# Optimization experiments

Hardware: AMD Instinct MI355X
Metric: run time of the kernel (lower is better)

Reference implementation:

```python
import jax, jax.numpy as jnp
import numpy as np

MAX_ABS = 1.0          # assumed get_max_abs('T')
DT = 0.01              # forward default dt
TWO_PI = 2.0 * np.pi
B, D, N = 4096, 2048, 4096


def setup_inputs() -> dict:
    key = jax.random.key(0)
    k0, k1 = jax.random.split(key, 2)
    x = jax.random.normal(k0, (B, D), dtype=jnp.float32)
    # nn.Linear params
    W = jax.random.normal(k1, (N, D), dtype=jnp.float32) * (1.0 / np.sqrt(D))
    b = jnp.zeros((N,), dtype=jnp.float32)
    # oscillator params (as initialized in __init__)
    amplitude = jnp.ones((N,), dtype=jnp.float32)
    frequency = jnp.ones((N,), dtype=jnp.float32)
    phase_offset = jnp.zeros((N,), dtype=jnp.float32)
    damping = jnp.full((N,), 0.01, dtype=jnp.float32)
    return {"x": x, "W": W, "b": b, "amplitude": amplitude,
            "frequency": frequency, "phase_offset": phase_offset,
            "damping": damping}


def reference(x, W, b, amplitude, frequency, phase_offset, damping):
    # driving force: [B, N]
    force = x @ W.T + b
    omega_sq = (TWO_PI * frequency) ** 2  # [N]
    # t starts at 0 and is incremented ONCE per forward call
    t = DT

    def step(carry, f):
        state, vel = carry
        accel = -omega_sq * state - damping * vel + f
        vel = vel + accel * DT
        state = state + vel * DT
        return (state, vel), state

    init = (jnp.zeros((N,), x.dtype), jnp.zeros((N,), x.dtype))
    (_, _), states = jax.lax.scan(step, init, force)  # states: [B, N]

    # sinusoid term is identical for every batch step (t fixed within forward)
    osc = amplitude * jnp.sin(TWO_PI * frequency * t + phase_offset)  # [N]
    out = jnp.clip(states + osc, -MAX_ABS, MAX_ABS)
    return out
```

## Files before the change

kernel.cpp:

```cpp
#include <hip/hip_runtime.h>
#include <hip/hip_bf16.h>
#include <math.h>

#define MDIM 4096
#define KDIM 2048
#define NDIM 4096
#define DT   0.01f
#define TWO_PI_F 6.283185307179586f
#define CH 64
#define CL 64
#define TILES (KDIM / 64)

typedef __attribute__((ext_vector_type(8))) short bf16x8;
typedef __attribute__((ext_vector_type(4))) float f32x4;

__device__ __forceinline__ unsigned short f2bf(float f) {
  unsigned int u = __float_as_uint(f);
  u += 0x7FFFu + ((u >> 16) & 1u);
  return (unsigned short)(u >> 16);
}
__device__ __forceinline__ float bf2f(unsigned short u) {
  return __uint_as_float(((unsigned int)u) << 16);
}

__global__ void cast2_bf16_kernel(const float* __restrict__ s0,
                                  unsigned short* __restrict__ d0,
                                  const float* __restrict__ s1,
                                  unsigned short* __restrict__ d1,
                                  int n4each) {
  int i = blockIdx.x * blockDim.x + threadIdx.x;
  const float4* sp;
  ushort4* dp;
  int j;
  if (i < n4each) { sp = (const float4*)s0; dp = (ushort4*)d0; j = i; }
  else            { sp = (const float4*)s1; dp = (ushort4*)d1; j = i - n4each; }
  float4 v = sp[j];
  ushort4 o;
  o.x = f2bf(v.x); o.y = f2bf(v.y); o.z = f2bf(v.z); o.w = f2bf(v.w);
  dp[j] = o;
}


__device__ __forceinline__ void gload16(const unsigned short* g,
                                        unsigned short* l) {
  __builtin_amdgcn_global_load_lds(
      (const __attribute__((address_space(1))) unsigned int*)g,
      (__attribute__((address_space(3))) unsigned int*)l, 16, 0, 0);
}

#define WAITVM(n) asm volatile("s_waitcnt vmcnt(" #n ")" ::: "memory")

__global__ __launch_bounds__(512, 2) void gemm_scan256_kernel(
    const unsigned short* __restrict__ A,
    const unsigned short* __restrict__ Bm,
    const float* __restrict__ bias,
    const float* __restrict__ freq,
    const float* __restrict__ damp,
    unsigned short* __restrict__ zpart,
    float* __restrict__ chunkS,
    float* __restrict__ chunkV) {
  extern __shared__ __align__(16) unsigned short smem[];

  const int tid  = threadIdx.x;
  const int lane = tid & 63;
  const int w    = tid >> 6;
  const int wr   = w >> 2;
  const int wc   = w & 3;
  const int q    = lane >> 4;
  const int lm   = lane & 15;

  const int bid = blockIdx.x;
  const int wg  = (bid & 7) * 32 + (bid >> 3);
  const int tm  = wg >> 4;
  const int tn  = wg & 15;
  const int bM  = tm * 256;
  const int bN  = tn * 256;

  const int srow  = w * 16 + (lane >> 2);
  const int sslot = (lane & 3) ^ ((lane >> 3) & 3);
  const unsigned short* gA = A  + (size_t)(bM + srow) * KDIM + sslot * 8;
  const unsigned short* gB = Bm + (size_t)(bN + srow) * KDIM + sslot * 8;
  const int ldst = w * 512 + lane * 8;

#define SUNIT(mat, u, ks, rh)                                              \
  gload16((mat ? gB : gA) + (size_t)(rh) * 128 * KDIM + (u) * 64 + (ks) * 32, \
          smem + ((u) & 1) * 32768 + (mat) * 16384 + (ks) * 8192 +         \
              (rh) * 4096 + ldst)

  const int flane = (lm >> 1) & 3;
  const int aoff  = (wr * 128 + lm) * 32 + ((q ^ flane) * 8);
  const int boff  = 16384 + (wc * 64 + lm) * 32 + ((q ^ flane) * 8);

  f32x4 acc[8][4];
#pragma unroll
  for (int i = 0; i < 8; i++)
#pragma unroll
    for (int j = 0; j < 4; j++) acc[i][j] = (f32x4){0.f, 0.f, 0.f, 0.f};

  SUNIT(1, 0, 0, 0); SUNIT(1, 0, 0, 1);
  SUNIT(0, 0, 0, 0); SUNIT(0, 0, 0, 1);
  SUNIT(1, 0, 1, 0); SUNIT(1, 0, 1, 1);
  SUNIT(0, 0, 1, 0); SUNIT(0, 0, 1, 1);
  SUNIT(1, 1, 0, 0); SUNIT(1, 1, 0, 1);
  SUNIT(0, 1, 0, 0); SUNIT(0, 1, 0, 1);
  SUNIT(1, 1, 1, 0); SUNIT(1, 1, 1, 1);

#define LDA(KS, MH)                                                        \
  _Pragma("unroll") for (int m = 0; m < 4; ++m) af[m] =                    \
      *(const bf16x8*)&smem[bufo + (KS) + (MH) + aoff + m * 512]
#define LDB(KS)                                                            \
  _Pragma("unroll") for (int n = 0; n < 4; ++n) bfv[n] =                   \
      *(const bf16x8*)&smem[bufo + (KS) + boff + n * 512]
#define MFMA16(MB)                                                         \
  __builtin_amdgcn_s_setprio(1);                                           \
  _Pragma("unroll") for (int m = 0; m < 4; ++m)                            \
      _Pragma("unroll") for (int n = 0; n < 4; ++n)                        \
          acc[(MB) + m][n] = __builtin_amdgcn_mfma_f32_16x16x32_bf16(      \
              af[m], bfv[n], acc[(MB) + m][n], 0, 0, 0);                   \
  __builtin_amdgcn_s_setprio(0)

#pragma unroll 2
  for (int t = 0; t < TILES; ++t) {
    const int bufo = (t & 1) * 32768;
    bf16x8 af[4], bfv[4];

    if (t < TILES - 1) WAITVM(10); else WAITVM(4);
    __builtin_amdgcn_s_barrier();
    LDA(0, 0);
    LDB(0);
    if (t + 1 < TILES) { SUNIT(0, t + 1, 1, 0); SUNIT(0, t + 1, 1, 1); }
    MFMA16(0);

    __builtin_amdgcn_s_barrier();
    LDA(0, 2048);
    if (t + 2 < TILES) { SUNIT(1, t + 2, 0, 0); SUNIT(1, t + 2, 0, 1); }
    MFMA16(4);

    if (t < TILES - 2) WAITVM(10);
    else if (t == TILES - 2) WAITVM(8);
    else WAITVM(0);
    __builtin_amdgcn_s_barrier();
    LDA(8192, 0);
    LDB(8192);
    if (t + 2 < TILES) { SUNIT(0, t + 2, 0, 0); SUNIT(0, t + 2, 0, 1); }
    MFMA16(0);

    __builtin_amdgcn_s_barrier();
    LDA(8192, 2048);
    if (t + 2 < TILES) { SUNIT(1, t + 2, 1, 0); SUNIT(1, t + 2, 1, 1); }
    MFMA16(4);
  }
#undef LDA
#undef LDB
#undef MFMA16
#undef SUNIT

  __syncthreads();

#pragma unroll
  for (int n = 0; n < 4; ++n) {
    const float bz = bias[bN + wc * 64 + n * 16 + lm];
#pragma unroll
    for (int M = 0; M < 8; ++M)
#pragma unroll
      for (int rr = 0; rr < 4; ++rr) {
        const int row = wr * 128 + M * 16 + q * 4 + rr;
        const int col = wc * 64 + ((n ^ q) * 16) + lm;
        smem[row * 256 + col] = f2bf(acc[M][n][rr] + bz);
      }
  }
  __syncthreads();

  {
    const int col  = tid & 255;
    const int ch0  = (tid >> 8) * 2;
    const int gcol = bN + col;
    const float om  = TWO_PI_F * freq[gcol];
    const float osq = om * om;
    const float dp  = damp[gcol];
#pragma unroll
    for (int cc = 0; cc < 2; ++cc) {
      const int ch = ch0 + cc;
      float s = 0.f, v = 0.f;
#pragma unroll 8
      for (int i = 0; i < CL; ++i) {
        const int row = ch * 64 + i;
        const int idx = row * 256 + (col ^ (((i >> 2) & 3) << 4));
        float f = bf2f(smem[idx]);
        v += (-osq * s - dp * v + f) * DT;
        s += v * DT;
        smem[idx] = f2bf(s);
      }
      const int chunk = tm * 4 + ch;
      chunkS[chunk * NDIM + gcol] = s;
      chunkV[chunk * NDIM + gcol] = v;
    }
  }
  __syncthreads();

#pragma unroll
  for (int k = 0; k < 16; ++k) {
    const int slot = tid + 512 * k;
    const int row  = slot >> 5;
    const int grp  = slot & 31;
    const int sgrp = grp ^ (((row >> 2) & 3) << 1);
    *(uint4*)&zpart[(size_t)(bM + row) * NDIM + bN + grp * 8] =
        *(const uint4*)&smem[row * 256 + sgrp * 8];
  }
}

__global__ void scan_pass2_inplace(float* __restrict__ chunkS,
                                   float* __restrict__ chunkV,
                                   const float* __restrict__ freq,
                                   const float* __restrict__ damp) {
  int n = blockIdx.x * blockDim.x + threadIdx.x;
  float om = TWO_PI_F * freq[n];
  float osq = om * om;
  float dp = damp[n];
  float a00 = 1.f - osq * DT * DT, a01 = DT * (1.f - dp * DT);
  float a10 = -osq * DT,           a11 = 1.f - dp * DT;
#pragma unroll
  for (int i = 0; i < 6; i++) {
    float b00 = a00 * a00 + a01 * a10;
    float b01 = a00 * a01 + a01 * a11;
    float b10 = a10 * a00 + a11 * a10;
    float b11 = a10 * a01 + a11 * a11;
    a00 = b00; a01 = b01; a10 = b10; a11 = b11;
  }
  float cs = 0.f, cv = 0.f;
#pragma unroll 8
  for (int c = 0; c < CH; c++) {
    float ls = chunkS[c * NDIM + n];
    float lv = chunkV[c * NDIM + n];
    chunkS[c * NDIM + n] = cs;
    chunkV[c * NDIM + n] = cv;
    float ns = a00 * cs + a01 * cv + ls;
    float nv = a10 * cs + a11 * cv + lv;
    cs = ns; cv = nv;
  }
}

__global__ void scan_out_carry4(const unsigned short* __restrict__ zpart,
                                const float* __restrict__ amp,
                                const float* __restrict__ freq,
                                const float* __restrict__ phase,
                                const float* __restrict__ damp,
                                const float* __restrict__ carryS,
                                const float* __restrict__ carryV,
                                float* __restrict__ out) {
  int gid = blockIdx.x * blockDim.x + threadIdx.x;
  int n4 = gid & (NDIM / 4 - 1);
  int cq = gid >> 10;
  int c  = cq >> 2;
  int qq = cq & 3;
  int n  = n4 * 4;

  float4 fr = *(const float4*)&freq[n];
  float4 dv = *(const float4*)&damp[n];
  float4 am = *(const float4*)&amp[n];
  float4 ph = *(const float4*)&phase[n];
  float omv[4] = {TWO_PI_F * fr.x, TWO_PI_F * fr.y, TWO_PI_F * fr.z, TWO_PI_F * fr.w};
  float dpv[4] = {dv.x, dv.y, dv.z, dv.w};
  float amv[4] = {am.x, am.y, am.z, am.w};
  float phv[4] = {ph.x, ph.y, ph.z, ph.w};
  float m00[4], m01[4], m10[4], m11[4], osc[4];
#pragma unroll
  for (int j = 0; j < 4; j++) {
    float osq = omv[j] * omv[j];
    m00[j] = 1.f - osq * DT * DT;  m01[j] = DT * (1.f - dpv[j] * DT);
    m10[j] = -osq * DT;            m11[j] = 1.f - dpv[j] * DT;
    osc[j] = amv[j] * sinf(omv[j] * DT + phv[j]);
  }

  float4 csv = *(const float4*)&carryS[c * NDIM + n];
  float4 cvv = *(const float4*)&carryV[c * NDIM + n];
  float cs[4] = {csv.x, csv.y, csv.z, csv.w};
  float cv[4] = {cvv.x, cvv.y, cvv.z, cvv.w};
  float hs[4], hv[4];
#pragma unroll
  for (int j = 0; j < 4; j++) {
    float p00 = m00[j], p01 = m01[j], p10 = m10[j], p11 = m11[j];
#pragma unroll
    for (int k = 0; k < 4; k++) {
      float b00 = p00 * p00 + p01 * p10;
      float b01 = p00 * p01 + p01 * p11;
      float b10 = p10 * p00 + p11 * p10;
      float b11 = p10 * p01 + p11 * p11;
      p00 = b00; p01 = b01; p10 = b10; p11 = b11;
    }
    float j00 = 1.f, j01 = 0.f, j10 = 0.f, j11 = 1.f;
    for (int k = 0; k < qq; k++) {
      float b00 = j00 * p00 + j01 * p10;
      float b01 = j00 * p01 + j01 * p11;
      float b10 = j10 * p00 + j11 * p10;
      float b11 = j10 * p01 + j11 * p11;
      j00 = b00; j01 = b01; j10 = b10; j11 = b11;
    }
    hs[j] = j00 * cs[j] + j01 * cv[j];
    hv[j] = j10 * cs[j] + j11 * cv[j];
  }

  const size_t r0 = (size_t)c * CL + qq * 16;
  const unsigned short* zp = zpart + r0 * NDIM + n;
  float* op = out + r0 * NDIM + n;
#pragma unroll 4
  for (int i = 0; i < 16; ++i) {
    ushort4 zv = *(const ushort4*)&zp[(size_t)i * NDIM];
    float z[4] = {bf2f(zv.x), bf2f(zv.y), bf2f(zv.z), bf2f(zv.w)};
    float o[4];
#pragma unroll
    for (int j = 0; j < 4; j++) {
      float t = m00[j] * hs[j] + m01[j] * hv[j];
      float u = m10[j] * hs[j] + m11[j] * hv[j];
      hs[j] = t; hv[j] = u;
      o[j] = fminf(1.f, fmaxf(-1.f, hs[j] + z[j] + osc[j]));
    }
    *(float4*)&op[(size_t)i * NDIM] = (float4){o[0], o[1], o[2], o[3]};
  }
}

__global__ __launch_bounds__(256, 2) void gemm_bt_kernel(
    const unsigned short* __restrict__ A,
    const unsigned short* __restrict__ Bm,
    const float* __restrict__ bias,
    unsigned short* __restrict__ C) {
  __shared__ __align__(16) unsigned short sA[128 * 32];
  __shared__ __align__(16) unsigned short sB[128 * 32];

  const int tid  = threadIdx.x;
  const int lane = tid & 63;
  const int wave = tid >> 6;
  const int wr = wave >> 1;
  const int wc = wave & 1;
  const int q  = lane >> 4;
  const int lm = lane & 15;

  const int bM = blockIdx.x * 128;
  const int bN = blockIdx.y * 128;

  f32x4 acc[4][4];
#pragma unroll
  for (int i = 0; i < 4; i++)
#pragma unroll
    for (int j = 0; j < 4; j++) acc[i][j] = (f32x4){0.f, 0.f, 0.f, 0.f};

  const int idx0 = tid;
  const int idx1 = tid + 256;
  const int r0 = idx0 >> 2, g0 = idx0 & 3;
  const int r1 = idx1 >> 2, g1 = idx1 & 3;
  const int dst0 = r0 * 32 + ((g0 ^ ((r0 >> 1) & 3)) * 8);
  const int dst1 = r1 * 32 + ((g1 ^ ((r1 >> 1) & 3)) * 8);
  const unsigned short* gA0 = A  + (size_t)(bM + r0) * KDIM + g0 * 8;
  const unsigned short* gA1 = A  + (size_t)(bM + r1) * KDIM + g1 * 8;
  const unsigned short* gB0 = Bm + (size_t)(bN + r0) * KDIM + g0 * 8;
  const unsigned short* gB1 = Bm + (size_t)(bN + r1) * KDIM + g1 * 8;
  const int rq = (q ^ ((lm >> 1) & 3)) * 8;

  for (int k0 = 0; k0 < KDIM; k0 += 32) {
    uint4 av0 = *(const uint4*)(gA0 + k0);
    uint4 av1 = *(const uint4*)(gA1 + k0);
    uint4 bv0 = *(const uint4*)(gB0 + k0);
    uint4 bv1 = *(const uint4*)(gB1 + k0);
    __syncthreads();
    *(uint4*)&sA[dst0] = av0;
    *(uint4*)&sA[dst1] = av1;
    *(uint4*)&sB[dst0] = bv0;
    *(uint4*)&sB[dst1] = bv1;
    __syncthreads();

    bf16x8 af[4], bfr[4];
#pragma unroll
    for (int mt = 0; mt < 4; mt++)
      af[mt]  = *(const bf16x8*)&sA[(wr * 64 + mt * 16 + lm) * 32 + rq];
#pragma unroll
    for (int nt = 0; nt < 4; nt++)
      bfr[nt] = *(const bf16x8*)&sB[(wc * 64 + nt * 16 + lm) * 32 + rq];

#pragma unroll
    for (int mt = 0; mt < 4; mt++)
#pragma unroll
      for (int nt = 0; nt < 4; nt++)
        acc[mt][nt] = __builtin_amdgcn_mfma_f32_16x16x32_bf16(
            af[mt], bfr[nt], acc[mt][nt], 0, 0, 0);
  }

#pragma unroll
  for (int nt = 0; nt < 4; nt++) {
    const int col = bN + wc * 64 + nt * 16 + lm;
    const float bz = bias[col];
#pragma unroll
    for (int mt = 0; mt < 4; mt++) {
      const int row0 = bM + wr * 64 + mt * 16 + q * 4;
#pragma unroll
      for (int r = 0; r < 4; r++)
        C[(size_t)(row0 + r) * NDIM + col] = f2bf(acc[mt][nt][r] + bz);
    }
  }
}

__global__ void scan_pass1(const unsigned short* __restrict__ force,
                           const float* __restrict__ freq,
                           const float* __restrict__ damp,
                           float* __restrict__ chunkS,
                           float* __restrict__ chunkV) {
  int gid = blockIdx.x * blockDim.x + threadIdx.x;
  int n4 = gid & (NDIM / 4 - 1);
  int c  = gid >> 10;
  int n  = n4 * 4;
  float4 fr = *(const float4*)&freq[n];
  float4 dv = *(const float4*)&damp[n];
  float osq[4] = {TWO_PI_F * fr.x, TWO_PI_F * fr.y, TWO_PI_F * fr.z, TWO_PI_F * fr.w};
  float dp[4]  = {dv.x, dv.y, dv.z, dv.w};
  float s[4] = {0.f, 0.f, 0.f, 0.f}, v[4] = {0.f, 0.f, 0.f, 0.f};
#pragma unroll
  for (int j = 0; j < 4; j++) osq[j] *= osq[j];
  const unsigned short* fp = force + (size_t)c * CL * NDIM + n;
#pragma unroll 4
  for (int i = 0; i < CL; i++) {
    ushort4 fv = *(const ushort4*)&fp[(size_t)i * NDIM];
    float f[4] = {bf2f(fv.x), bf2f(fv.y), bf2f(fv.z), bf2f(fv.w)};
#pragma unroll
    for (int j = 0; j < 4; j++) {
      float a = -osq[j] * s[j] - dp[j] * v[j] + f[j];
      v[j] += a * DT;
      s[j] += v[j] * DT;
    }
  }
  *(float4*)&chunkS[c * NDIM + n] = (float4){s[0], s[1], s[2], s[3]};
  *(float4*)&chunkV[c * NDIM + n] = (float4){v[0], v[1], v[2], v[3]};
}

__global__ void scan_pass2(const float* __restrict__ chunkS,
                           const float* __restrict__ chunkV,
                           const float* __restrict__ freq,
                           const float* __restrict__ damp,
                           float* __restrict__ carryS,
                           float* __restrict__ carryV) {
  int n = blockIdx.x * blockDim.x + threadIdx.x;
  float om = TWO_PI_F * freq[n];
  float osq = om * om;
  float dp = damp[n];
  float a00 = 1.f - osq * DT * DT, a01 = DT * (1.f - dp * DT);
  float a10 = -osq * DT,           a11 = 1.f - dp * DT;
#pragma unroll
  for (int i = 0; i < 6; i++) {
    float b00 = a00 * a00 + a01 * a10;
    float b01 = a00 * a01 + a01 * a11;
    float b10 = a10 * a00 + a11 * a10;
    float b11 = a10 * a01 + a11 * a11;
    a00 = b00; a01 = b01; a10 = b10; a11 = b11;
  }
  float cs = 0.f, cv = 0.f;
#pragma unroll 8
  for (int c = 0; c < CH; c++) {
    carryS[c * NDIM + n] = cs;
    carryV[c * NDIM + n] = cv;
    float ls = chunkS[c * NDIM + n];
    float lv = chunkV[c * NDIM + n];
    float ns = a00 * cs + a01 * cv + ls;
    float nv = a10 * cs + a11 * cv + lv;
    cs = ns; cv = nv;
  }
}

__global__ void scan_pass3(const unsigned short* __restrict__ force,
                           const float* __restrict__ amp,
                           const float* __restrict__ freq,
                           const float* __restrict__ phase,
                           const float* __restrict__ damp,
                           const float* __restrict__ carryS,
                           const float* __restrict__ carryV,
                           float* __restrict__ out) {
  int gid = blockIdx.x * blockDim.x + threadIdx.x;
  int n4 = gid & (NDIM / 4 - 1);
  int c  = gid >> 10;
  int n  = n4 * 4;
  float4 fr = *(const float4*)&freq[n];
  float4 dv = *(const float4*)&damp[n];
  float4 am = *(const float4*)&amp[n];
  float4 ph = *(const float4*)&phase[n];
  float om[4] = {TWO_PI_F * fr.x, TWO_PI_F * fr.y, TWO_PI_F * fr.z, TWO_PI_F * fr.w};
  float dp[4] = {dv.x, dv.y, dv.z, dv.w};
  float osq[4], osc[4], s[4], v[4];
  float amv[4] = {am.x, am.y, am.z, am.w};
  float phv[4] = {ph.x, ph.y, ph.z, ph.w};
#pragma unroll
  for (int j = 0; j < 4; j++) {
    osq[j] = om[j] * om[j];
    osc[j] = amv[j] * sinf(om[j] * DT + phv[j]);
  }
  float4 csv = *(const float4*)&carryS[c * NDIM + n];
  float4 cvv = *(const float4*)&carryV[c * NDIM + n];
  s[0] = csv.x; s[1] = csv.y; s[2] = csv.z; s[3] = csv.w;
  v[0] = cvv.x; v[1] = cvv.y; v[2] = cvv.z; v[3] = cvv.w;
  const unsigned short* fp = force + (size_t)c * CL * NDIM + n;
  float* op = out + (size_t)c * CL * NDIM + n;
#pragma unroll 4
  for (int i = 0; i < CL; i++) {
    ushort4 fv = *(const ushort4*)&fp[(size_t)i * NDIM];
    float f[4] = {bf2f(fv.x), bf2f(fv.y), bf2f(fv.z), bf2f(fv.w)};
    float o[4];
#pragma unroll
    for (int j = 0; j < 4; j++) {
      float a = -osq[j] * s[j] - dp[j] * v[j] + f[j];
      v[j] += a * DT;
      s[j] += v[j] * DT;
      o[j] = fminf(1.f, fmaxf(-1.f, s[j] + osc[j]));
    }
    *(float4*)&op[(size_t)i * NDIM] = (float4){o[0], o[1], o[2], o[3]};
  }
}

extern "C" void kernel_launch(void* const* d_in, const int* in_sizes, int n_in,
                              void* d_out, int out_size, void* d_ws, size_t ws_size,
                              hipStream_t stream) {
  const float* x     = (const float*)d_in[0];
  const float* W     = (const float*)d_in[1];
  const float* bias  = (const float*)d_in[2];
  const float* amp   = (const float*)d_in[3];
  const float* freq  = (const float*)d_in[4];
  const float* phase = (const float*)d_in[5];
  const float* damp  = (const float*)d_in[6];

  const size_t MiB = 1024 * 1024;
  const int n4each = MDIM * KDIM / 4;

  if (ws_size >= 66 * MiB) {
    unsigned short* xbf   = (unsigned short*)d_ws;
    unsigned short* wbf   = xbf + (size_t)MDIM * KDIM;
    unsigned short* zpart = wbf + (size_t)NDIM * KDIM;
    float* chunkS = (float*)((char*)d_ws + 64 * MiB);
    float* chunkV = chunkS + CH * NDIM;

    static bool attr_done = false;
    if (!attr_done) {
      (void)hipFuncSetAttribute((const void*)gemm_scan256_kernel,
                                hipFuncAttributeMaxDynamicSharedMemorySize,
                                131072);
      attr_done = true;
    }

    cast2_bf16_kernel<<<(2 * n4each + 255) / 256, 256, 0, stream>>>(
        x, xbf, W, wbf, n4each);
    gemm_scan256_kernel<<<dim3(256), dim3(512), 131072, stream>>>(
        xbf, wbf, bias, freq, damp, zpart, chunkS, chunkV);
    scan_pass2_inplace<<<NDIM / 256, 256, 0, stream>>>(chunkS, chunkV,
                                                       freq, damp);
    scan_out_carry4<<<CH * 4 * NDIM / 4 / 256, 256, 0, stream>>>(
        zpart, amp, freq, phase, damp, chunkS, chunkV, (float*)d_out);
  } else {
    dim3 gg(MDIM / 128, NDIM / 128);
    unsigned short* xbf   = (unsigned short*)d_ws;
    unsigned short* wbf   = xbf + (size_t)MDIM * KDIM;
    unsigned short* force = wbf + (size_t)NDIM * KDIM;
    float* chunkS = (float*)d_ws;
    float* chunkV = chunkS + CH * NDIM;
    float* carryS = chunkV + CH * NDIM;
    float* carryV = carryS + CH * NDIM;

    cast2_bf16_kernel<<<(2 * n4each + 255) / 256, 256, 0, stream>>>(
        x, xbf, W, wbf, n4each);
    gemm_bt_kernel<<<gg, 256, 0, stream>>>(xbf, wbf, bias, force);
    scan_pass1<<<CH * NDIM / 4 / 256, 256, 0, stream>>>(force, freq, damp,
                                                        chunkS, chunkV);
    scan_pass2<<<NDIM / 256, 256, 0, stream>>>(chunkS, chunkV, freq, damp,
                                               carryS, carryV);
    scan_pass3<<<CH * NDIM / 4 / 256, 256, 0, stream>>>(
        force, amp, freq, phase, damp, carryS, carryV, (float*)d_out);
  }
}
```

Baseline: 207.5 us.

## Double-buffer LDS fragments in registers to overlap ds_reads with MFMA

Restructures the GEMM main loop so the A/B fragments for the next MFMA group are read from LDS into a second register set while the current group's MFMAs execute. It uses explicit lgkmcnt waits and sched_barriers to keep the compiler from reordering. The vmcnt waits are rebalanced around the new stage layout. This hides LDS read latency but doubles fragment registers, which risks pressure at 512 threads x2 occupancy, and it makes the barrier/wait-count ordering more fragile.

After: 256.0 us. +23.3%, slower.

```diff
diff --git a/kernel.cpp b/kernel.cpp
--- a/kernel.cpp
+++ b/kernel.cpp
@@ -49,6 +49,8 @@
 }
 
 #define WAITVM(n) asm volatile("s_waitcnt vmcnt(" #n ")" ::: "memory")
+#define WAITLGKM(n) asm volatile("s_waitcnt lgkmcnt(" #n ")" ::: "memory")
+#define SCHEDB() __builtin_amdgcn_sched_barrier(0)
 
 __global__ __launch_bounds__(512, 2) void gemm_scan256_kernel(
     const unsigned short* __restrict__ A,
@@ -105,53 +107,67 @@
   SUNIT(0, 1, 0, 0); SUNIT(0, 1, 0, 1);
   SUNIT(1, 1, 1, 0); SUNIT(1, 1, 1, 1);
 
-#define LDA(KS, MH)                                                        \
-  _Pragma("unroll") for (int m = 0; m < 4; ++m) af[m] =                    \
-      *(const bf16x8*)&smem[bufo + (KS) + (MH) + aoff + m * 512]
-#define LDB(KS)                                                            \
-  _Pragma("unroll") for (int n = 0; n < 4; ++n) bfv[n] =                   \
-      *(const bf16x8*)&smem[bufo + (KS) + boff + n * 512]
-#define MFMA16(MB)                                                         \
-  __builtin_amdgcn_s_setprio(1);                                           \
+#define LDA4(dst, BUFO, KS, MH)                                            \
+  _Pragma("unroll") for (int m = 0; m < 4; ++m) dst[m] =                   \
+      *(const bf16x8*)&smem[(BUFO) + (KS) + (MH) + aoff + m * 512]
+#define LDB4(dst, BUFO, KS)                                                \
+  _Pragma("unroll") for (int n = 0; n < 4; ++n) dst[n] =                   \
+      *(const bf16x8*)&smem[(BUFO) + (KS) + boff + n * 512]
+#define MFMA16(AF, BF, MB)                                                 \
+  __builtin_amdgcn_s_setprio(1);                                          \
   _Pragma("unroll") for (int m = 0; m < 4; ++m)                            \
       _Pragma("unroll") for (int n = 0; n < 4; ++n)                        \
           acc[(MB) + m][n] = __builtin_amdgcn_mfma_f32_16x16x32_bf16(      \
-              af[m], bfv[n], acc[(MB) + m][n], 0, 0, 0);                   \
+              AF[m], BF[n], acc[(MB) + m][n], 0, 0, 0);                    \
   __builtin_amdgcn_s_setprio(0)
+
+  bf16x8 af0[4], af1[4], bf0[4], bf1[4];
+
+  WAITVM(10);
+  __builtin_amdgcn_s_barrier();
+  LDA4(af0, 0, 0, 0);
+  LDB4(bf0, 0, 0);
 
 #pragma unroll 2
   for (int t = 0; t < TILES; ++t) {
-    const int bufo = (t & 1) * 32768;
-    bf16x8 af[4], bfv[4];
-
-    if (t < TILES - 1) WAITVM(10); else WAITVM(4);
+    const int bufo  = (t & 1) * 32768;
+    const int nbufo = ((t + 1) & 1) * 32768;
+
     __builtin_amdgcn_s_barrier();
-    LDA(0, 0);
-    LDB(0);
     if (t + 1 < TILES) { SUNIT(0, t + 1, 1, 0); SUNIT(0, t + 1, 1, 1); }
-    MFMA16(0);
-
+    LDA4(af1, bufo, 0, 2048);
+    WAITLGKM(4); SCHEDB();
+    MFMA16(af0, bf0, 0);
+
+    if (t < TILES - 1) { WAITVM(8); } else { WAITVM(0); }
     __builtin_amdgcn_s_barrier();
-    LDA(0, 2048);
     if (t + 2 < TILES) { SUNIT(1, t + 2, 0, 0); SUNIT(1, t + 2, 0, 1); }
-    MFMA16(4);
-
-    if (t < TILES - 2) WAITVM(10);
-    else if (t == TILES - 2) WAITVM(8);
-    else WAITVM(0);
+    LDA4(af0, bufo, 8192, 0);
+    LDB4(bf1, bufo, 8192);
+    WAITLGKM(8); SCHEDB();
+    MFMA16(af1, bf0, 4);
+
     __builtin_amdgcn_s_barrier();
-    LDA(8192, 0);
-    LDB(8192);
     if (t + 2 < TILES) { SUNIT(0, t + 2, 0, 0); SUNIT(0, t + 2, 0, 1); }
-    MFMA16(0);
-
+    LDA4(af1, bufo, 8192, 2048);
+    WAITLGKM(4); SCHEDB();
+    MFMA16(af0, bf1, 0);
+
+    if (t < TILES - 2) { WAITVM(8); }
+    else if (t == TILES - 2) { WAITVM(4); }
     __builtin_amdgcn_s_barrier();
-    LDA(8192, 2048);
     if (t + 2 < TILES) { SUNIT(1, t + 2, 1, 0); SUNIT(1, t + 2, 1, 1); }
-    MFMA16(4);
-  }
-#undef LDA
-#undef LDB
+    if (t + 1 < TILES) {
+      LDA4(af0, nbufo, 0, 0);
+      LDB4(bf0, nbufo, 0);
+      WAITLGKM(8); SCHEDB();
+    } else {
+      WAITLGKM(0); SCHEDB();
+    }
+    MFMA16(af1, bf1, 4);
+  }
+#undef LDA4
+#undef LDB4
 #undef MFMA16
 #undef SUNIT
 
```
